# Kernel optimization log

Hardware: AMD Instinct MI355X
Metric: run time of the kernel (lower is better)

## Reference

```python
import jax, jax.numpy as jnp
import numpy as np

H = 4      # attention heads
C = 64     # hidden_dim per head
GAT_SLOPE = 0.2   # PyG GATConv leaky_relu negative_slope
ACT_SLOPE = 0.01  # nn.LeakyReLU / F.leaky_relu default


def gat_layer(x, src, dst, W, a_src, a_dst, b, n):
    # x: [n, F_in] -> h: [n, H, C]
    h = (x @ W).reshape(n, H, C)
    al_s = jnp.einsum('nhc,hc->nh', h, a_src)  # [n, H]
    al_d = jnp.einsum('nhc,hc->nh', h, a_dst)
    e = jax.nn.leaky_relu(al_s[src] + al_d[dst], GAT_SLOPE)  # [E, H]
    # segment softmax over destination nodes (self-loops ensure non-empty segments)
    m = jax.ops.segment_max(e, dst, num_segments=n)
    p = jnp.exp(e - m[dst])
    s = jax.ops.segment_sum(p, dst, num_segments=n)
    alpha = p / s[dst]
    out = jax.ops.segment_sum(h[src] * alpha[:, :, None], dst, num_segments=n)  # [n, H, C]
    return out.reshape(n, H * C) + b


def setup_inputs() -> dict:
    key = jax.random.key(0)
    ks = jax.random.split(key, 24)
    N, E = 102400, 409600
    F_IN, F_OUT = 80, 80
    HC = H * C
    RIN, RHID, ROUT = 60, 512, 60
    def g(k, shape, scale):
        return (jax.random.normal(k, shape, dtype=jnp.float32) * scale)
    inp = {
        'x': g(ks[0], (N, F_IN), 1.0),
        'edge_index': jax.random.randint(ks[1], (2, E), 0, N, dtype=jnp.int64),
        'root_ctx_norm': g(ks[2], (4096, RIN), 1.0),
        'W0': g(ks[3], (F_IN, HC), 0.1), 'a_src0': g(ks[4], (H, C), 0.1), 'a_dst0': g(ks[5], (H, C), 0.1), 'b0': jnp.zeros((HC,), jnp.float32),
        'W1': g(ks[6], (HC, HC), 0.06), 'a_src1': g(ks[7], (H, C), 0.1), 'a_dst1': g(ks[8], (H, C), 0.1), 'b1': jnp.zeros((HC,), jnp.float32),
        'W2': g(ks[9], (HC, HC), 0.06), 'a_src2': g(ks[10], (H, C), 0.1), 'a_dst2': g(ks[11], (H, C), 0.1), 'b2': jnp.zeros((HC,), jnp.float32),
        'fc_w': g(ks[12], (HC, F_OUT), 0.06), 'fc_b': jnp.zeros((F_OUT,), jnp.float32),
        'r_w1': g(ks[13], (RIN, RHID), 0.1), 'r_b1': jnp.zeros((RHID,), jnp.float32),
        'r_w2': g(ks[14], (RHID, RHID), 0.04), 'r_b2': jnp.zeros((RHID,), jnp.float32),
        'r_w3': g(ks[15], (RHID, ROUT), 0.04), 'r_b3': jnp.zeros((ROUT,), jnp.float32),
    }
    return inp


def reference(x, edge_index, root_ctx_norm,
              W0, a_src0, a_dst0, b0,
              W1, a_src1, a_dst1, b1,
              W2, a_src2, a_dst2, b2,
              fc_w, fc_b, r_w1, r_b1, r_w2, r_b2, r_w3, r_b3):
    n = x.shape[0]
    loops = jnp.arange(n, dtype=edge_index.dtype)
    src = jnp.concatenate([edge_index[0], loops])  # PyG add_self_loops=True
    dst = jnp.concatenate([edge_index[1], loops])
    h = gat_layer(x, src, dst, W0, a_src0, a_dst0, b0, n)
    h = jax.nn.leaky_relu(h, ACT_SLOPE)  # dropout is identity in eval
    h = gat_layer(h, src, dst, W1, a_src1, a_dst1, b1, n)
    h = jax.nn.leaky_relu(h, ACT_SLOPE)
    h = gat_layer(h, src, dst, W2, a_src2, a_dst2, b2, n)
    rot = h @ fc_w + fc_b
    r = jax.nn.leaky_relu(root_ctx_norm @ r_w1 + r_b1, ACT_SLOPE)
    r = jax.nn.leaky_relu(r @ r_w2 + r_b2, ACT_SLOPE)
    root_norm = r @ r_w3 + r_b3
    return rot, root_norm
```

## Files before the change

### kernel.cpp

```cpp
#include <hip/hip_runtime.h>
#include <hip/hip_bf16.h>


#define GAT_SLOPE 0.2f
#define ACT_SLOPE 0.01f

typedef unsigned short ushort_t;
typedef __attribute__((ext_vector_type(8))) short bf16x8;
typedef __attribute__((ext_vector_type(8))) unsigned short ushort8v;
typedef __attribute__((ext_vector_type(4))) unsigned short ushort4v;
typedef __attribute__((ext_vector_type(4))) float floatx4;

__device__ __forceinline__ float lrelu(float x, float s) {
    return fmaxf(x, s * x);
}

__device__ __forceinline__ ushort_t f2bf(float f) {
    union { float f; unsigned u; } x; x.f = f;
    unsigned r = x.u + 0x7FFF + ((x.u >> 16) & 1);
    return (ushort_t)(r >> 16);
}

__device__ __forceinline__ float bf2f(ushort_t u) {
    union { unsigned u; float f; } x; x.u = ((unsigned)u) << 16;
    return x.f;
}

__device__ __forceinline__ void gl_lds16(const ushort_t* g, ushort_t* l) {
    __builtin_amdgcn_global_load_lds(
        (const __attribute__((address_space(1))) unsigned int*)g,
        (__attribute__((address_space(3))) unsigned int*)l, 16, 0, 0);
}

__global__ void detect_fmt(const int* __restrict__ raw, int nwords, int* flag) {
    __shared__ int nz;
    if (threadIdx.x == 0) nz = 0;
    __syncthreads();
    int lim = nwords < 4096 ? nwords : 4096;
    for (int i = threadIdx.x * 2 + 1; i < lim; i += 512)
        if (raw[i] != 0) atomicAdd(&nz, 1);
    __syncthreads();
    if (threadIdx.x == 0) *flag = (nz == 0) ? 1 : 0;
}

__global__ void zero2(int* __restrict__ a, int* __restrict__ b, int n) {
    int i = blockIdx.x * blockDim.x + threadIdx.x;
    if (i < n) { a[i] = 0; b[i] = 0; }
}

__global__ void convert_count(const int* __restrict__ raw, int E,
                              const int* __restrict__ flag,
                              int* __restrict__ idx32, int* __restrict__ counts) {
    int i = blockIdx.x * blockDim.x + threadIdx.x;
    if (i >= E) return;
    int f = *flag;
    int s = f ? raw[2 * i] : raw[i];
    int d = f ? raw[2 * (E + i)] : raw[E + i];
    idx32[i] = s;
    idx32[E + i] = d;
    atomicAdd(&counts[d], 1);
}

__global__ void scan_block(const int* __restrict__ counts, int* __restrict__ inc,
                           int* __restrict__ blockSums, int N) {
    __shared__ int sh[256];
    int i = blockIdx.x * 256 + threadIdx.x;
    int v = (i < N) ? counts[i] : 0;
    sh[threadIdx.x] = v;
    __syncthreads();
    for (int off = 1; off < 256; off <<= 1) {
        int t = (threadIdx.x >= off) ? sh[threadIdx.x - off] : 0;
        __syncthreads();
        sh[threadIdx.x] += t;
        __syncthreads();
    }
    if (i < N) inc[i] = sh[threadIdx.x];
    if (threadIdx.x == 255) blockSums[blockIdx.x] = sh[255];
}

__global__ void scan_sums(int* __restrict__ blockSums, int nb, int* __restrict__ row_ptr) {
    __shared__ int sh[512];
    int v = ((int)threadIdx.x < nb) ? blockSums[threadIdx.x] : 0;
    sh[threadIdx.x] = v;
    __syncthreads();
    for (int off = 1; off < 512; off <<= 1) {
        int t = (threadIdx.x >= off) ? sh[threadIdx.x - off] : 0;
        __syncthreads();
        sh[threadIdx.x] += t;
        __syncthreads();
    }
    if ((int)threadIdx.x < nb) blockSums[threadIdx.x] = sh[threadIdx.x];
    if (threadIdx.x == 0) row_ptr[0] = 0;
}

__global__ void scan_add(const int* __restrict__ inc, const int* __restrict__ blockSums,
                         int* __restrict__ row_ptr, int N) {
    int i = blockIdx.x * 256 + threadIdx.x;
    if (i < N) row_ptr[i + 1] = inc[i] + (blockIdx.x > 0 ? blockSums[blockIdx.x - 1] : 0);
}

__global__ void edge_fill(const int* __restrict__ src, const int* __restrict__ dst, int E,
                          const int* __restrict__ row_ptr, int* __restrict__ cursor,
                          int* __restrict__ col) {
    int i = blockIdx.x * blockDim.x + threadIdx.x;
    if (i < E) {
        int d = dst[i];
        int pos = row_ptr[d] + atomicAdd(&cursor[d], 1);
        col[pos] = src[i];
    }
}

__global__ void convert_padrow(const float* __restrict__ in, ushort_t* __restrict__ out,
                               int M, int Kr, int Kp) {
    int i = blockIdx.x * blockDim.x + threadIdx.x;
    if (i >= M * Kp) return;
    int r = i / Kp, c = i - r * Kp;
    out[i] = f2bf((c < Kr) ? in[(size_t)r * Kr + c] : 0.f);
}

struct WConv { const float* in; ushort_t* out; int Kp, Kr, N, Npad, blkOff; };
struct WConvArr { WConv e[7]; int n; };

__global__ void convert_w_multi(WConvArr a) {
    int b = blockIdx.x;
    int ei = 0;
    for (int k = 1; k < a.n; k++)
        if (b >= a.e[k].blkOff) ei = k;
    WConv w = a.e[ei];
    int i = (b - w.blkOff) * 256 + threadIdx.x;
    if (i >= w.Npad * w.Kp) return;
    int n = i / w.Kp, k = i - n * w.Kp;
    float v = (n < w.N && k < w.Kr) ? w.in[(size_t)k * w.N + n] : 0.f;
    w.out[i] = f2bf(v);
}

__global__ __launch_bounds__(256) void gemm_gat(
    const ushort_t* __restrict__ A, const ushort_t* __restrict__ Bt,
    const float* __restrict__ a_src, const float* __restrict__ a_dst,
    ushort_t* __restrict__ Hbf, float* __restrict__ al_s, float* __restrict__ al_d,
    int M, int K) {
    __shared__ __align__(16) ushort_t As[2][128 * 32];
    __shared__ __align__(16) ushort_t Bs[2][128 * 32];
    int t = threadIdx.x;
    int wave = t >> 6, lane = t & 63;
    int wm = (wave >> 1) << 6;
    int wn = (wave & 1) << 6;
    int rowBase = blockIdx.y << 7;
    int colBase = blockIdx.x << 7;
    int lrow = lane & 15, lquad = lane >> 4;
    floatx4 acc[4][4];
#pragma unroll
    for (int i = 0; i < 4; i++)
#pragma unroll
        for (int j = 0; j < 4; j++) acc[i][j] = (floatx4){0.f, 0.f, 0.f, 0.f};

    int c0 = wave * 64 + lane;
    const ushort_t* gA0 = A + (size_t)(rowBase + (c0 >> 2)) * K + ((c0 & 3) << 3);
    const ushort_t* gB0 = Bt + (size_t)(colBase + (c0 >> 2)) * K + ((c0 & 3) << 3);
    int c1 = 256 + c0;
    const ushort_t* gA1 = A + (size_t)(rowBase + (c1 >> 2)) * K + ((c1 & 3) << 3);
    const ushort_t* gB1 = Bt + (size_t)(colBase + (c1 >> 2)) * K + ((c1 & 3) << 3);
    const int ldsOff0 = (wave * 64) * 8;
    const int ldsOff1 = (256 + wave * 64) * 8;

    const int nt = K >> 5;
#define STAGE_GAT(tt, b)                          \
    do {                                          \
        int k0_ = (tt) << 5;                      \
        gl_lds16(gA0 + k0_, &As[b][ldsOff0]);     \
        gl_lds16(gA1 + k0_, &As[b][ldsOff1]);     \
        gl_lds16(gB0 + k0_, &Bs[b][ldsOff0]);     \
        gl_lds16(gB1 + k0_, &Bs[b][ldsOff1]);     \
    } while (0)

    STAGE_GAT(0, 0);
    STAGE_GAT(1, 1);
    asm volatile("s_waitcnt vmcnt(4)" ::: "memory");
    __builtin_amdgcn_s_barrier();

    for (int kt = 0; kt < nt; ++kt) {
        int b = kt & 1;
        bf16x8 af[4], bfv[4];
#pragma unroll
        for (int i = 0; i < 4; i++)
            af[i] = *(const bf16x8*)(&As[b][(wm + i * 16 + lrow) * 32 + lquad * 8]);
#pragma unroll
        for (int j = 0; j < 4; j++)
            bfv[j] = *(const bf16x8*)(&Bs[b][(wn + j * 16 + lrow) * 32 + lquad * 8]);
        asm volatile("s_waitcnt lgkmcnt(0)" ::: "memory");
        __builtin_amdgcn_sched_barrier(0);
        __builtin_amdgcn_s_barrier();
        bool more = (kt + 2) < nt;
        if (more) STAGE_GAT(kt + 2, b);
#pragma unroll
        for (int i = 0; i < 4; i++)
#pragma unroll
            for (int j = 0; j < 4; j++)
                acc[i][j] = __builtin_amdgcn_mfma_f32_16x16x32_bf16(af[i], bfv[j],
                                                                    acc[i][j], 0, 0, 0);
        if (more)
            asm volatile("s_waitcnt vmcnt(4)" ::: "memory");
        else
            asm volatile("s_waitcnt vmcnt(0)" ::: "memory");
        __builtin_amdgcn_s_barrier();
        __builtin_amdgcn_sched_barrier(0);
    }
#undef STAGE_GAT

    int head = (colBase + wn) >> 6;
    float avs[4], avd[4];
#pragma unroll
    for (int j = 0; j < 4; j++) {
        avs[j] = a_src[head * 64 + j * 16 + lrow];
        avd[j] = a_dst[head * 64 + j * 16 + lrow];
    }
#pragma unroll
    for (int i = 0; i < 4; i++) {
#pragma unroll
        for (int r = 0; r < 4; r++) {
            float ps = 0.f, pd = 0.f;
#pragma unroll
            for (int j = 0; j < 4; j++) {
                ps += acc[i][j][r] * avs[j];
                pd += acc[i][j][r] * avd[j];
            }
#pragma unroll
            for (int off = 1; off < 16; off <<= 1) {
                ps += __shfl_xor(ps, off);
                pd += __shfl_xor(pd, off);
            }
            if (lrow == 0) {
                int gr = rowBase + wm + i * 16 + lquad * 4 + r;
                al_s[gr * 4 + head] = ps;
                al_d[gr * 4 + head] = pd;
            }
        }
        int grb = rowBase + wm + i * 16 + lquad * 4;
#pragma unroll
        for (int j = 0; j < 4; j++) {
            int gc = colBase + wn + j * 16 + lrow;
#pragma unroll
            for (int r = 0; r < 4; r++)
                Hbf[(size_t)(grb + r) * 256 + gc] = f2bf(acc[i][j][r]);
        }
    }
}

__global__ __launch_bounds__(256) void gemm_plain(
    const ushort_t* __restrict__ A, const ushort_t* __restrict__ Bt,
    const float* __restrict__ bias, void* __restrict__ Cout,
    int M, int N, int K, int act, float slope, int outBf) {
    __shared__ __align__(16) ushort_t As[2][128 * 32];
    __shared__ __align__(16) ushort_t Bs[2][128 * 32];
    int t = threadIdx.x;
    int wave = t >> 6, lane = t & 63;
    int wm = (wave >> 1) << 6;
    int wn = (wave & 1) << 6;
    int rowBase = blockIdx.y << 7;
    int colBase = blockIdx.x << 7;
    int lrow = lane & 15, lquad = lane >> 4;
    floatx4 acc[4][4];
#pragma unroll
    for (int i = 0; i < 4; i++)
#pragma unroll
        for (int j = 0; j < 4; j++) acc[i][j] = (floatx4){0.f, 0.f, 0.f, 0.f};

    int c0 = wave * 64 + lane;
    const ushort_t* gA0 = A + (size_t)(rowBase + (c0 >> 2)) * K + ((c0 & 3) << 3);
    const ushort_t* gB0 = Bt + (size_t)(colBase + (c0 >> 2)) * K + ((c0 & 3) << 3);
    int c1 = 256 + c0;
    const ushort_t* gA1 = A + (size_t)(rowBase + (c1 >> 2)) * K + ((c1 & 3) << 3);
    const ushort_t* gB1 = Bt + (size_t)(colBase + (c1 >> 2)) * K + ((c1 & 3) << 3);
    const int ldsOff0 = (wave * 64) * 8;
    const int ldsOff1 = (256 + wave * 64) * 8;

    const int nt = K >> 5;
#define STAGE_PLN(tt, b)                          \
    do {                                          \
        int k0_ = (tt) << 5;                      \
        gl_lds16(gA0 + k0_, &As[b][ldsOff0]);     \
        gl_lds16(gA1 + k0_, &As[b][ldsOff1]);     \
        gl_lds16(gB0 + k0_, &Bs[b][ldsOff0]);     \
        gl_lds16(gB1 + k0_, &Bs[b][ldsOff1]);     \
    } while (0)

    STAGE_PLN(0, 0);
    STAGE_PLN(1, 1);
    asm volatile("s_waitcnt vmcnt(4)" ::: "memory");
    __builtin_amdgcn_s_barrier();

    for (int kt = 0; kt < nt; ++kt) {
        int b = kt & 1;
        bf16x8 af[4], bfv[4];
#pragma unroll
        for (int i = 0; i < 4; i++)
            af[i] = *(const bf16x8*)(&As[b][(wm + i * 16 + lrow) * 32 + lquad * 8]);
#pragma unroll
        for (int j = 0; j < 4; j++)
            bfv[j] = *(const bf16x8*)(&Bs[b][(wn + j * 16 + lrow) * 32 + lquad * 8]);
        asm volatile("s_waitcnt lgkmcnt(0)" ::: "memory");
        __builtin_amdgcn_sched_barrier(0);
        __builtin_amdgcn_s_barrier();
        bool more = (kt + 2) < nt;
        if (more) STAGE_PLN(kt + 2, b);
#pragma unroll
        for (int i = 0; i < 4; i++)
#pragma unroll
            for (int j = 0; j < 4; j++)
                acc[i][j] = __builtin_amdgcn_mfma_f32_16x16x32_bf16(af[i], bfv[j],
                                                                    acc[i][j], 0, 0, 0);
        if (more)
            asm volatile("s_waitcnt vmcnt(4)" ::: "memory");
        else
            asm volatile("s_waitcnt vmcnt(0)" ::: "memory");
        __builtin_amdgcn_s_barrier();
        __builtin_amdgcn_sched_barrier(0);
    }
#undef STAGE_PLN

#pragma unroll
    for (int i = 0; i < 4; i++) {
        int gr = rowBase + wm + i * 16 + lquad * 4;
#pragma unroll
        for (int j = 0; j < 4; j++) {
            int gc = colBase + wn + j * 16 + lrow;
            if (gc >= N) continue;
            float b = bias ? bias[gc] : 0.f;
#pragma unroll
            for (int r = 0; r < 4; r++) {
                float v = acc[i][j][r] + b;
                if (act) v = lrelu(v, slope);
                if (outBf)
                    ((ushort_t*)Cout)[(size_t)(gr + r) * N + gc] = f2bf(v);
                else
                    ((float*)Cout)[(size_t)(gr + r) * N + gc] = v;
            }
        }
    }
}

__global__ __launch_bounds__(256) void gat_agg(
    const ushort_t* __restrict__ h_bf, const float* __restrict__ al_s,
    const float* __restrict__ al_d, const int* __restrict__ row_ptr,
    const int* __restrict__ col, const float* __restrict__ bias,
    ushort_t* __restrict__ out_bf, int N, int act, float slope) {
    int wid = (blockIdx.x * 256 + threadIdx.x) >> 6;
    int lane = threadIdx.x & 63;
    int half = lane >> 5;
    int lane8 = lane & 31;
    int n = wid * 2 + half;
    if (n >= N) return;
    int head = lane8 >> 3;
    int idx4 = n * 4 + head;
    float ad = al_d[idx4];
    const ushort8v* h8 = (const ushort8v*)h_bf;
    float p = __expf(lrelu(al_s[idx4] + ad, GAT_SLOPE));
    ushort8v hv = h8[(size_t)n * 32 + lane8];
    float s = p;
    float acc[8];
#pragma unroll
    for (int c = 0; c < 8; c++) acc[c] = p * bf2f(hv[c]);
    int beg = row_ptr[n], end = row_ptr[n + 1];
    for (int i = beg; i < end; i += 4) {
        int cnt = end - i;
        int sn0 = col[i];
        int sn1 = (cnt > 1) ? col[i + 1] : sn0;
        int sn2 = (cnt > 2) ? col[i + 2] : sn0;
        int sn3 = (cnt > 3) ? col[i + 3] : sn0;
        ushort8v h0 = h8[(size_t)sn0 * 32 + lane8];
        ushort8v h1 = h8[(size_t)sn1 * 32 + lane8];
        ushort8v h2 = h8[(size_t)sn2 * 32 + lane8];
        ushort8v h3 = h8[(size_t)sn3 * 32 + lane8];
        float a0 = al_s[sn0 * 4 + head];
        float a1 = al_s[sn1 * 4 + head];
        float a2 = al_s[sn2 * 4 + head];
        float a3 = al_s[sn3 * 4 + head];
        float p0 = __expf(lrelu(a0 + ad, GAT_SLOPE));
#pragma unroll
        for (int c = 0; c < 8; c++) acc[c] += p0 * bf2f(h0[c]);
        s += p0;
        if (cnt > 1) {
            float p1 = __expf(lrelu(a1 + ad, GAT_SLOPE));
#pragma unroll
            for (int c = 0; c < 8; c++) acc[c] += p1 * bf2f(h1[c]);
            s += p1;
        }
        if (cnt > 2) {
            float p2 = __expf(lrelu(a2 + ad, GAT_SLOPE));
#pragma unroll
            for (int c = 0; c < 8; c++) acc[c] += p2 * bf2f(h2[c]);
            s += p2;
        }
        if (cnt > 3) {
            float p3 = __expf(lrelu(a3 + ad, GAT_SLOPE));
#pragma unroll
            for (int c = 0; c < 8; c++) acc[c] += p3 * bf2f(h3[c]);
            s += p3;
        }
    }
    float rs = 1.f / s;
    const float4* b4 = (const float4*)bias;
    float4 b0 = b4[lane8 * 2];
    float4 b1 = b4[lane8 * 2 + 1];
    float bv[8] = {b0.x, b0.y, b0.z, b0.w, b1.x, b1.y, b1.z, b1.w};
    ushort8v o;
#pragma unroll
    for (int c = 0; c < 8; c++) {
        float v = acc[c] * rs + bv[c];
        if (act) v = lrelu(v, slope);
        o[c] = f2bf(v);
    }
    ((ushort8v*)out_bf)[(size_t)n * 32 + lane8] = o;
}

extern "C" void kernel_launch(void* const* d_in, const int* in_sizes, int n_in,
                              void* d_out, int out_size, void* d_ws, size_t ws_size,
                              hipStream_t stream) {
    const float* x        = (const float*)d_in[0];
    const int*   rawEdge  = (const int*)d_in[1];
    const float* rootCtx  = (const float*)d_in[2];
    const float* W[3]     = {(const float*)d_in[3], (const float*)d_in[7], (const float*)d_in[11]};
    const float* aS[3]    = {(const float*)d_in[4], (const float*)d_in[8], (const float*)d_in[12]};
    const float* aD[3]    = {(const float*)d_in[5], (const float*)d_in[9], (const float*)d_in[13]};
    const float* bb[3]    = {(const float*)d_in[6], (const float*)d_in[10], (const float*)d_in[14]};
    const float* fc_w     = (const float*)d_in[15];
    const float* fc_b     = (const float*)d_in[16];
    const float* r_w1     = (const float*)d_in[17];
    const float* r_b1     = (const float*)d_in[18];
    const float* r_w2     = (const float*)d_in[19];
    const float* r_b2     = (const float*)d_in[20];
    const float* r_w3     = (const float*)d_in[21];
    const float* r_b3     = (const float*)d_in[22];

    const int N  = in_sizes[0] / 80;
    const int E  = in_sizes[1] / 2;
    const int R  = in_sizes[2] / 60;
    const int N4 = N * 4;

    float* outRot  = (float*)d_out;
    float* outRoot = (float*)d_out + (size_t)N * 80;

    size_t off = 0;
    auto carve = [&](size_t bytes) -> void* {
        off = (off + 255) & ~(size_t)255;
        void* p = (char*)d_ws + off;
        off += bytes;
        return p;
    };
    int*      flag      = (int*)carve(4);
    int*      idx32     = (int*)carve((size_t)2 * E * 4);
    int*      counts    = (int*)carve((size_t)N * 4);
    int*      cursor    = (int*)carve((size_t)N * 4);
    int*      row_ptr   = (int*)carve((size_t)(N + 1) * 4);
    int*      incArr    = (int*)carve((size_t)N * 4);
    int*      blockSums = (int*)carve(512 * 4);
    int*      colArr    = (int*)carve((size_t)E * 4);
    float*    al_s      = (float*)carve((size_t)N4 * 4);
    float*    al_d      = (float*)carve((size_t)N4 * 4);
    ushort_t* h_bf      = (ushort_t*)carve((size_t)N * 256 * 2);
    ushort_t* agg_bf    = (ushort_t*)carve((size_t)N * 256 * 2);
    ushort_t* x_bf      = (ushort_t*)carve((size_t)N * 96 * 2);
    ushort_t* rc_bf     = (ushort_t*)carve((size_t)R * 64 * 2);
    ushort_t* t1_bf     = (ushort_t*)carve((size_t)R * 512 * 2);
    ushort_t* t2_bf     = (ushort_t*)carve((size_t)R * 512 * 2);
    ushort_t* Wt0       = (ushort_t*)carve((size_t)256 * 96 * 2);
    ushort_t* Wt1       = (ushort_t*)carve((size_t)256 * 256 * 2);
    ushort_t* Wt2       = (ushort_t*)carve((size_t)256 * 256 * 2);
    ushort_t* fcWt      = (ushort_t*)carve((size_t)128 * 256 * 2);
    ushort_t* rW1t      = (ushort_t*)carve((size_t)512 * 64 * 2);
    ushort_t* rWt2      = (ushort_t*)carve((size_t)512 * 512 * 2);
    ushort_t* rWt3      = (ushort_t*)carve((size_t)128 * 512 * 2);

    const int nb = (N + 255) / 256;
    dim3 blk(256);

    detect_fmt<<<1, 256, 0, stream>>>(rawEdge, 2 * E, flag);
    zero2<<<(N + 255) / 256, blk, 0, stream>>>(counts, cursor, N);
    convert_count<<<(E + 255) / 256, blk, 0, stream>>>(rawEdge, E, flag, idx32, counts);
    const int* srcArr = idx32;
    const int* dstArr = idx32 + E;
    scan_block<<<nb, 256, 0, stream>>>(counts, incArr, blockSums, N);
    scan_sums<<<1, 512, 0, stream>>>(blockSums, nb, row_ptr);
    scan_add<<<nb, 256, 0, stream>>>(incArr, blockSums, row_ptr, N);
    edge_fill<<<(E + 255) / 256, blk, 0, stream>>>(srcArr, dstArr, E, row_ptr, cursor, colArr);

    {
        WConvArr wa;
        auto mk = [&](int i, const float* in, ushort_t* out, int Kp, int Kr, int Nn, int Npad,
                      int blkOff) {
            wa.e[i] = WConv{in, out, Kp, Kr, Nn, Npad, blkOff};
        };
        int boff = 0;
        auto nblk = [](int Npad, int Kp) { return (Npad * Kp + 255) / 256; };
        mk(0, W[0], Wt0, 96, 80, 256, 256, boff);   boff += nblk(256, 96);
        mk(1, W[1], Wt1, 256, 256, 256, 256, boff); boff += nblk(256, 256);
        mk(2, W[2], Wt2, 256, 256, 256, 256, boff); boff += nblk(256, 256);
        mk(3, fc_w, fcWt, 256, 256, 80, 128, boff); boff += nblk(128, 256);
        mk(4, r_w1, rW1t, 64, 60, 512, 512, boff);  boff += nblk(512, 64);
        mk(5, r_w2, rWt2, 512, 512, 512, 512, boff); boff += nblk(512, 512);
        mk(6, r_w3, rWt3, 512, 512, 60, 128, boff);  boff += nblk(128, 512);
        wa.n = 7;
        convert_w_multi<<<boff, blk, 0, stream>>>(wa);
    }
    convert_padrow<<<(N * 96 + 255) / 256, blk, 0, stream>>>(x, x_bf, N, 80, 96);
    convert_padrow<<<(R * 64 + 255) / 256, blk, 0, stream>>>(rootCtx, rc_bf, R, 60, 64);

    const int aggBlocks = (N / 2 + 3) / 4;
    const ushort_t* curA = x_bf;
    int curK = 96;
    for (int l = 0; l < 3; l++) {
        dim3 g1(2, N / 128);
        gemm_gat<<<g1, blk, 0, stream>>>(curA, l == 0 ? Wt0 : (l == 1 ? Wt1 : Wt2),
                                         aS[l], aD[l], h_bf, al_s, al_d, N, curK);
        int act = (l < 2) ? 1 : 0;
        gat_agg<<<aggBlocks, blk, 0, stream>>>(h_bf, al_s, al_d, row_ptr,
                                               colArr, bb[l], agg_bf, N,
                                               act, ACT_SLOPE);
        curA = agg_bf;
        curK = 256;
    }

    {
        dim3 g(1, N / 128);
        gemm_plain<<<g, blk, 0, stream>>>(agg_bf, fcWt, fc_b, outRot, N, 80, 256,
                                          0, 0.f, 0);
    }
    {
        dim3 g1(512 / 128, R / 128);
        gemm_plain<<<g1, blk, 0, stream>>>(rc_bf, rW1t, r_b1, t1_bf, R, 512, 64,
                                           1, ACT_SLOPE, 1);
        dim3 g2(512 / 128, R / 128);
        gemm_plain<<<g2, blk, 0, stream>>>(t1_bf, rWt2, r_b2, t2_bf, R, 512, 512,
                                           1, ACT_SLOPE, 1);
        dim3 g3(1, R / 128);
        gemm_plain<<<g3, blk, 0, stream>>>(t2_bf, rWt3, r_b3, outRoot, R, 60, 512,
                                           0, 0.f, 0);
    }
}
```

Baseline: 514.8 us.

## Load entire K extent into LDS up front, drop double-buffered pipeline

Replaces the double-buffered LDS staging loop with a single pass that issues all global-to-LDS loads for the full K dimension (up to 8 tiles), then one barrier, then a compute loop with no per-iteration waits or barriers. The intent is to remove per-tile synchronization overhead, since K is at most 256. The cost is a much larger LDS footprint (128 KB for A and B together), which reduces occupancy and serializes all loads ahead of compute.

Measured after the change: 595.8 us. 15.7% more time.

```diff
diff --git a/kernel.cpp b/kernel.cpp
--- a/kernel.cpp
+++ b/kernel.cpp
@@ -139,8 +139,8 @@
     const float* __restrict__ a_src, const float* __restrict__ a_dst,
     ushort_t* __restrict__ Hbf, float* __restrict__ al_s, float* __restrict__ al_d,
     int M, int K) {
-    __shared__ __align__(16) ushort_t As[2][128 * 32];
-    __shared__ __align__(16) ushort_t Bs[2][128 * 32];
+    __shared__ __align__(16) ushort_t As[8 * 128 * 32];
+    __shared__ __align__(16) ushort_t Bs[8 * 128 * 32];
     int t = threadIdx.x;
     int wave = t >> 6, lane = t & 63;
     int wm = (wave >> 1) << 6;
@@ -164,48 +164,33 @@
     const int ldsOff1 = (256 + wave * 64) * 8;
 
     const int nt = K >> 5;
-#define STAGE_GAT(tt, b)                          \
-    do {                                          \
-        int k0_ = (tt) << 5;                      \
-        gl_lds16(gA0 + k0_, &As[b][ldsOff0]);     \
-        gl_lds16(gA1 + k0_, &As[b][ldsOff1]);     \
-        gl_lds16(gB0 + k0_, &Bs[b][ldsOff0]);     \
-        gl_lds16(gB1 + k0_, &Bs[b][ldsOff1]);     \
-    } while (0)
-
-    STAGE_GAT(0, 0);
-    STAGE_GAT(1, 1);
-    asm volatile("s_waitcnt vmcnt(4)" ::: "memory");
-    __builtin_amdgcn_s_barrier();
-
     for (int kt = 0; kt < nt; ++kt) {
-        int b = kt & 1;
+        int k0 = kt << 5;
+        int ldsT = kt << 12;
+        gl_lds16(gA0 + k0, &As[ldsT + ldsOff0]);
+        gl_lds16(gA1 + k0, &As[ldsT + ldsOff1]);
+        gl_lds16(gB0 + k0, &Bs[ldsT + ldsOff0]);
+        gl_lds16(gB1 + k0, &Bs[ldsT + ldsOff1]);
+    }
+    __syncthreads();
+
+    for (int kt = 0; kt < nt; ++kt) {
+        const ushort_t* At = &As[kt << 12];
+        const ushort_t* Bl = &Bs[kt << 12];
         bf16x8 af[4], bfv[4];
 #pragma unroll
         for (int i = 0; i < 4; i++)
-            af[i] = *(const bf16x8*)(&As[b][(wm + i * 16 + lrow) * 32 + lquad * 8]);
+            af[i] = *(const bf16x8*)(At + (wm + i * 16 + lrow) * 32 + lquad * 8);
 #pragma unroll
         for (int j = 0; j < 4; j++)
-            bfv[j] = *(const bf16x8*)(&Bs[b][(wn + j * 16 + lrow) * 32 + lquad * 8]);
-        asm volatile("s_waitcnt lgkmcnt(0)" ::: "memory");
-        __builtin_amdgcn_sched_barrier(0);
-        __builtin_amdgcn_s_barrier();
-        bool more = (kt + 2) < nt;
-        if (more) STAGE_GAT(kt + 2, b);
+            bfv[j] = *(const bf16x8*)(Bl + (wn + j * 16 + lrow) * 32 + lquad * 8);
 #pragma unroll
         for (int i = 0; i < 4; i++)
 #pragma unroll
             for (int j = 0; j < 4; j++)
                 acc[i][j] = __builtin_amdgcn_mfma_f32_16x16x32_bf16(af[i], bfv[j],
                                                                     acc[i][j], 0, 0, 0);
-        if (more)
-            asm volatile("s_waitcnt vmcnt(4)" ::: "memory");
-        else
-            asm volatile("s_waitcnt vmcnt(0)" ::: "memory");
-        __builtin_amdgcn_s_barrier();
-        __builtin_amdgcn_sched_barrier(0);
-    }
-#undef STAGE_GAT
+    }
 
     int head = (colBase + wn) >> 6;
     float avs[4], avd[4];
```

## Stage GAT GEMM tiles through registers instead of direct global-to-LDS loads

Applied to the files above, without the earlier changes.

Replaces the asynchronous global-to-LDS copies in the GAT projection GEMM with an explicit register-staged pipeline. Each iteration writes the previously loaded tile from registers into the other LDS buffer, issues global loads for tile kt+2, then runs MFMAs on the current buffer, with one barrier per iteration instead of two. This trades LDS-DMA for extra VGPR pressure and relies on the compiler's implicit vmcnt waits before the register writes, which may stall on global latency earlier than before.

New measurement: 509.5 us. No clear change (-1.0%).

```diff
diff --git a/kernel.cpp b/kernel.cpp
--- a/kernel.cpp
+++ b/kernel.cpp
@@ -160,26 +160,37 @@
     int c1 = 256 + c0;
     const ushort_t* gA1 = A + (size_t)(rowBase + (c1 >> 2)) * K + ((c1 & 3) << 3);
     const ushort_t* gB1 = Bt + (size_t)(colBase + (c1 >> 2)) * K + ((c1 & 3) << 3);
-    const int ldsOff0 = (wave * 64) * 8;
-    const int ldsOff1 = (256 + wave * 64) * 8;
+    const int wsl0 = (wave * 64 + lane) * 8;
+    const int wsl1 = (256 + wave * 64 + lane) * 8;
 
     const int nt = K >> 5;
-#define STAGE_GAT(tt, b)                          \
-    do {                                          \
-        int k0_ = (tt) << 5;                      \
-        gl_lds16(gA0 + k0_, &As[b][ldsOff0]);     \
-        gl_lds16(gA1 + k0_, &As[b][ldsOff1]);     \
-        gl_lds16(gB0 + k0_, &Bs[b][ldsOff0]);     \
-        gl_lds16(gB1 + k0_, &Bs[b][ldsOff1]);     \
+    ushort8v rA0, rA1, rB0, rB1;
+#define LOADR(tt)                                     \
+    do {                                              \
+        int k0_ = (tt) << 5;                          \
+        rA0 = *(const ushort8v*)(gA0 + k0_);          \
+        rA1 = *(const ushort8v*)(gA1 + k0_);          \
+        rB0 = *(const ushort8v*)(gB0 + k0_);          \
+        rB1 = *(const ushort8v*)(gB1 + k0_);          \
     } while (0)
-
-    STAGE_GAT(0, 0);
-    STAGE_GAT(1, 1);
-    asm volatile("s_waitcnt vmcnt(4)" ::: "memory");
+#define WRITER(b)                                     \
+    do {                                              \
+        *(ushort8v*)(&As[b][wsl0]) = rA0;             \
+        *(ushort8v*)(&As[b][wsl1]) = rA1;             \
+        *(ushort8v*)(&Bs[b][wsl0]) = rB0;             \
+        *(ushort8v*)(&Bs[b][wsl1]) = rB1;             \
+    } while (0)
+
+    LOADR(0);
+    WRITER(0);
+    LOADR(1);
+    asm volatile("s_waitcnt lgkmcnt(0)" ::: "memory");
     __builtin_amdgcn_s_barrier();
 
     for (int kt = 0; kt < nt; ++kt) {
         int b = kt & 1;
+        if (kt + 1 < nt) WRITER(b ^ 1);
+        if (kt + 2 < nt) LOADR(kt + 2);
         bf16x8 af[4], bfv[4];
 #pragma unroll
         for (int i = 0; i < 4; i++)
@@ -187,25 +198,17 @@
 #pragma unroll
         for (int j = 0; j < 4; j++)
             bfv[j] = *(const bf16x8*)(&Bs[b][(wn + j * 16 + lrow) * 32 + lquad * 8]);
-        asm volatile("s_waitcnt lgkmcnt(0)" ::: "memory");
-        __builtin_amdgcn_sched_barrier(0);
-        __builtin_amdgcn_s_barrier();
-        bool more = (kt + 2) < nt;
-        if (more) STAGE_GAT(kt + 2, b);
 #pragma unroll
         for (int i = 0; i < 4; i++)
 #pragma unroll
             for (int j = 0; j < 4; j++)
                 acc[i][j] = __builtin_amdgcn_mfma_f32_16x16x32_bf16(af[i], bfv[j],
                                                                     acc[i][j], 0, 0, 0);
-        if (more)
-            asm volatile("s_waitcnt vmcnt(4)" ::: "memory");
-        else
-            asm volatile("s_waitcnt vmcnt(0)" ::: "memory");
+        asm volatile("s_waitcnt lgkmcnt(0)" ::: "memory");
         __builtin_amdgcn_s_barrier();
-        __builtin_amdgcn_sched_barrier(0);
-    }
-#undef STAGE_GAT
+    }
+#undef LOADR
+#undef WRITER
 
     int head = (colBase + wn) >> 6;
     float avs[4], avd[4];
```
